# Kernel tuning notes

Measured on AMD Instinct MI355X. Metric: run time of the kernel, lower is better.

The kernel has to match this reference:

```python
import jax, jax.numpy as jnp
import numpy as np

H, W = 256, 256
FRONT_K = 8
ALPHA_T = 1.0 / 255.0
EPS = 1e-8               # transmittance early-stop threshold (meta_f32[4])
BG = (0.0, 0.0, 0.0)     # background color
CHUNK = 128              # gaussians composited per scan step


def setup_inputs() -> dict:
    key = jax.random.key(0)
    k1, k2, k3, k4, k5, k6, k7 = jax.random.split(key, 7)
    B, G = 2, 8192
    # gaussian centers spread over the image plane
    means2d = jax.random.uniform(k1, (B, G, 2), jnp.float32) * jnp.array([W, H], jnp.float32)
    # positive-definite conics (inverse 2D covariance): a, c > 0, |b| < sqrt(a*c)
    a = 0.05 + 0.45 * jax.random.uniform(k2, (B, G), jnp.float32)
    c = 0.05 + 0.45 * jax.random.uniform(k3, (B, G), jnp.float32)
    b = 0.5 * (jax.random.uniform(k4, (B, G), jnp.float32) - 0.5) * jnp.sqrt(a * c)
    conics = jnp.stack([a, b, c], axis=-1)
    colors = jax.random.uniform(k5, (B, G, 3), jnp.float32)
    opacities = jax.random.uniform(k6, (B, G), jnp.float32)
    depths = jax.random.uniform(k7, (B, G), jnp.float32) * 10.0
    return {"means2d": means2d, "conics": conics, "colors": colors,
            "opacities": opacities, "depths": depths}


def _rasterize_one(means2d, conics, colors, opacities, depths):
    # depth sort (stable, front-to-back)
    perm = jnp.argsort(depths, stable=True)
    m = means2d[perm]      # [G,2]
    co = conics[perm]      # [G,3]
    col = colors[perm]     # [G,3]
    op = opacities[perm]   # [G]
    G = m.shape[0]
    n_chunks = G // CHUNK

    px = jnp.arange(W, dtype=jnp.float32) + 0.5  # pixel centers
    py = jnp.arange(H, dtype=jnp.float32) + 0.5
    bg = jnp.asarray(BG, jnp.float32)

    def step(carry, chunk):
        accum, T, count = carry                    # [H,W,3], [H,W], [H,W] int32
        mC, coC, colC, opC = chunk                 # [K,2],[K,3],[K,3],[K]
        dx = px[None, None, :] - mC[:, 0][:, None, None]   # [K,1,W]
        dy = py[None, :, None] - mC[:, 1][:, None, None]   # [K,H,1]
        a = coC[:, 0][:, None, None]
        b = coC[:, 1][:, None, None]
        c = coC[:, 2][:, None, None]
        sigma = 0.5 * (a * dx * dx + c * dy * dy) + b * dx * dy  # [K,H,W]
        alpha = jnp.minimum(opC[:, None, None] * jnp.exp(-sigma), 0.999)
        alpha = jnp.where((sigma >= 0.0) & (alpha >= ALPHA_T), alpha, 0.0)
        kept = (alpha > 0.0).astype(jnp.int32)
        # front_k: only the first FRONT_K contributing gaussians per pixel
        before = count[None] + jnp.cumsum(kept, axis=0) - kept
        alpha = jnp.where(before < FRONT_K, alpha, 0.0)
        kept = (alpha > 0.0).astype(jnp.int32)
        one_m = 1.0 - alpha
        cp = jnp.cumprod(one_m, axis=0)                              # [K,H,W]
        Tc = T[None] * jnp.concatenate([jnp.ones((1, H, W), alpha.dtype), cp[:-1]], 0)
        w = jnp.where(Tc > EPS, Tc * alpha, 0.0)                     # early-stop gate
        accum = accum + jnp.einsum('khw,kc->hwc', w, colC)
        T = T * cp[-1]
        count = count + jnp.sum(kept, axis=0)
        return (accum, T, count), None

    chunks = (m.reshape(n_chunks, CHUNK, 2),
              co.reshape(n_chunks, CHUNK, 3),
              col.reshape(n_chunks, CHUNK, 3),
              op.reshape(n_chunks, CHUNK))
    init = (jnp.zeros((H, W, 3), jnp.float32),
            jnp.ones((H, W), jnp.float32),
            jnp.zeros((H, W), jnp.int32))
    (accum, T, _), _ = jax.lax.scan(step, init, chunks)
    return accum + T[..., None] * bg


def reference(means2d, conics, colors, opacities, depths):
    return jax.vmap(_rasterize_one)(means2d, conics, colors, opacities, depths)
```

## Files before the change

### kernel.cpp

```cpp
#include <hip/hip_runtime.h>
#include <math.h>

#define GN 8192
#define BN 2
#define HN 256
#define WN 256
#define FRONT_K 8
#define EPS_T 1e-8f
#define ALPHA_T (1.0f / 255.0f)
#define TDIM 32
#define NTILE (TDIM * TDIM)
#define CAP 256

__global__ __launch_bounds__(64) void pgr_clear(unsigned* __restrict__ cur)
{
    cur[blockIdx.x * 64 + threadIdx.x] = 0u;
}

__global__ __launch_bounds__(64) void pgr_prep(
    const float* __restrict__ means2d, const float* __restrict__ conics,
    const float* __restrict__ colors, const float* __restrict__ opac,
    const float* __restrict__ depths,
    unsigned* __restrict__ cur, unsigned long long* __restrict__ kent,
    float4* __restrict__ recA, float4* __restrict__ recB,
    float* __restrict__ recC)
{
    int g = blockIdx.x * 64 + threadIdx.x;
    int b = g >> 13, i = g & (GN - 1);
    float2 mxy = reinterpret_cast<const float2*>(means2d)[g];
    float mx = mxy.x, my = mxy.y;
    float ca = conics[3 * g], cb = conics[3 * g + 1], cc = conics[3 * g + 2];
    float r = colors[3 * g], g2 = colors[3 * g + 1], b3 = colors[3 * g + 2];
    float op = opac[g];
    float dep = depths[g];

    float s = (op > 0.f) ? (__logf(255.0f * op) + 1e-4f) : -1.0f;
    if (s < 0.f) return;
    float det = fmaxf(ca * cc - cb * cb, 1e-12f);
    float dxm = sqrtf(2.f * s * cc / det) + 0.02f;
    float dym = sqrtf(2.f * s * ca / det) + 0.02f;
    int x0 = (int)floorf(mx - dxm - 0.5f), x1 = (int)ceilf(mx + dxm - 0.5f);
    int y0 = (int)floorf(my - dym - 0.5f), y1 = (int)ceilf(my + dym - 0.5f);
    if (x1 < 0 || x0 > WN - 1 || y1 < 0 || y0 > HN - 1) return;
    x0 = max(x0, 0); x1 = min(x1, WN - 1);
    y0 = max(y0, 0); y1 = min(y1, HN - 1);
    int tx0 = x0 >> 3, tx1 = x1 >> 3, ty0 = y0 >> 3, ty1 = y1 >> 3;

    unsigned long long key =
        ((unsigned long long)__float_as_uint(dep) << 13) | (unsigned)i;
    float4 A = make_float4(mx, my, ca, cb);
    float4 B = make_float4(cc, op, r, g2);

    for (int ty = ty0; ty <= ty1; ++ty)
        for (int tx = tx0; tx <= tx1; ++tx) {
            int t = b * NTILE + ty * TDIM + tx;
            unsigned pos = atomicAdd(&cur[t], 1u);
            if (pos < CAP) {
                int sl = t * CAP + (int)pos;
                kent[sl] = key;
                recA[sl] = A;
                recB[sl] = B;
                recC[sl] = b3;
            }
        }
}

__device__ __forceinline__ int rank_of(const unsigned long long* s_key,
                                       unsigned long long k, int L)
{
    int rank = 0, j = 0;
    for (; j + 4 <= L; j += 4) {
        unsigned long long k0 = s_key[j], k1 = s_key[j + 1];
        unsigned long long k2 = s_key[j + 2], k3 = s_key[j + 3];
        rank += (int)(k0 < k) + (int)(k1 < k) + (int)(k2 < k) + (int)(k3 < k);
    }
    for (; j < L; ++j) rank += (int)(s_key[j] < k);
    return rank;
}

__global__ __launch_bounds__(64) void pgr_raster(
    const unsigned* __restrict__ cur, const unsigned long long* __restrict__ kent,
    const float4* __restrict__ recA, const float4* __restrict__ recB,
    const float* __restrict__ recC, float* __restrict__ out)
{
    const int b = blockIdx.z;
    const int t = b * NTILE + blockIdx.y * TDIM + blockIdx.x;
    const int tid = threadIdx.x;
    const int tx0 = blockIdx.x * 8, ty0 = blockIdx.y * 8;
    const int lx = tid & 7, ly = tid >> 3;
    const float px = tx0 + lx + 0.5f, py = ty0 + ly + 0.5f;

    __shared__ unsigned long long s_key[CAP];
    __shared__ float4 s_d0[CAP], s_d1[CAP];
    __shared__ float s_d2[CAP];

    const int base = t * CAP;
    unsigned long long myk = kent[base + tid];
    float4 r0 = recA[base + tid];
    float4 r1 = recB[base + tid];
    float r2 = recC[base + tid];
    const int L = min((int)cur[t], CAP);

    if (tid < L) s_key[tid] = myk;
    for (int i = 64 + tid; i < L; i += 64)
        s_key[i] = kent[base + i];
    __syncthreads();

    if (tid < L) {
        int rank = rank_of(s_key, myk, L);
        s_d0[rank] = r0; s_d1[rank] = r1; s_d2[rank] = r2;
    }
    for (int i = 64 + tid; i < L; i += 64) {
        int rank = rank_of(s_key, s_key[i], L);
        s_d0[rank] = recA[base + i];
        s_d1[rank] = recB[base + i];
        s_d2[rank] = recC[base + i];
    }
    __syncthreads();

    float accR = 0.f, accG = 0.f, accB = 0.f, T = 1.f;
    int count = 0;
    bool done = false;

    for (int i0 = 0; i0 < L; i0 += 8) {
        if (__all((int)done)) break;
        float alpha[8], colR[8], colG[8], colB[8];
        bool valid[8];
        #pragma unroll
        for (int k = 0; k < 8; ++k) {
            int idx = i0 + k;
            bool act = (idx < L) && !done;
            int ii = act ? idx : i0;
            float4 d0 = s_d0[ii];
            float4 d1 = s_d1[ii];
            float dx = __fsub_rn(px, d0.x);
            float dy = __fsub_rn(py, d0.y);
            float t1 = __fmul_rn(__fmul_rn(d0.z, dx), dx);
            float t2 = __fmul_rn(__fmul_rn(d1.x, dy), dy);
            float sigma = __fadd_rn(__fmul_rn(0.5f, __fadd_rn(t1, t2)),
                                    __fmul_rn(__fmul_rn(d0.w, dx), dy));
            bool v = act && sigma >= 0.f && sigma <= 5.55f;
            float al = v ? fminf(__fmul_rn(d1.y, __expf(-sigma)), 0.999f) : 0.f;
            valid[k] = v && (al >= ALPHA_T);
            alpha[k] = al;
            colR[k] = d1.z; colG[k] = d1.w; colB[k] = s_d2[ii];
        }
        #pragma unroll
        for (int k = 0; k < 8; ++k) {
            if (valid[k] && !done) {
                float al = alpha[k];
                if (T > EPS_T) {
                    float w = __fmul_rn(T, al);
                    accR += w * colR[k];
                    accG += w * colG[k];
                    accB += w * colB[k];
                }
                T = __fmul_rn(T, __fsub_rn(1.f, al));
                count++;
                if (count >= FRONT_K || T <= EPS_T) done = true;
            }
        }
    }

    int o = ((b * HN + (ty0 + ly)) * WN + (tx0 + lx)) * 3;
    out[o] = accR;
    out[o + 1] = accG;
    out[o + 2] = accB;
}

extern "C" void kernel_launch(void* const* d_in, const int* in_sizes, int n_in,
                              void* d_out, int out_size, void* d_ws, size_t ws_size,
                              hipStream_t stream) {
    const float* means2d = (const float*)d_in[0];
    const float* conics  = (const float*)d_in[1];
    const float* colors  = (const float*)d_in[2];
    const float* opac    = (const float*)d_in[3];
    const float* depths  = (const float*)d_in[4];
    float* out = (float*)d_out;

    const int NSLOT = BN * NTILE * CAP;
    float4*             recA = (float4*)d_ws;
    float4*             recB = recA + NSLOT;
    unsigned long long* kent = (unsigned long long*)(recB + NSLOT);
    float*              recC = (float*)(kent + NSLOT);
    unsigned*           cur  = (unsigned*)(recC + NSLOT);

    pgr_clear<<<(BN * NTILE) / 64, 64, 0, stream>>>(cur);
    pgr_prep<<<(BN * GN) / 64, 64, 0, stream>>>(means2d, conics, colors, opac,
                                                depths, cur, kent, recA, recB, recC);
    pgr_raster<<<dim3(TDIM, TDIM, BN), 64, 0, stream>>>(
        cur, kent, recA, recB, recC, out);
}
```

Measured before the change: 47.91 us.

## Split per-tile gaussian evaluation across four waves with bitmask compositing

The raster block grows from one wave to four. Each thread now loads one sorted entry, so loading and ranking run in a single pass instead of a loop. Each wave tests a quarter of the tile's depth-sorted list and records which gaussians pass the alpha test in a 64-bit mask per pixel. Wave 0 then walks those masks in order and composites only the first FRONT_K contributors, recomputing their alpha. This trades the original early exit for more parallel evaluation across all entries, plus extra sync and a serial tail in one wave.

```diff
diff --git a/kernel.cpp b/kernel.cpp
--- a/kernel.cpp
+++ b/kernel.cpp
@@ -78,7 +78,7 @@
     return rank;
 }
 
-__global__ __launch_bounds__(64) void pgr_raster(
+__global__ __launch_bounds__(256) void pgr_raster(
     const unsigned* __restrict__ cur, const unsigned long long* __restrict__ kent,
     const float4* __restrict__ recA, const float4* __restrict__ recB,
     const float* __restrict__ recC, float* __restrict__ out)
@@ -86,13 +86,15 @@
     const int b = blockIdx.z;
     const int t = b * NTILE + blockIdx.y * TDIM + blockIdx.x;
     const int tid = threadIdx.x;
+    const int wave = tid >> 6, lane = tid & 63;
     const int tx0 = blockIdx.x * 8, ty0 = blockIdx.y * 8;
-    const int lx = tid & 7, ly = tid >> 3;
+    const int lx = lane & 7, ly = lane >> 3;
     const float px = tx0 + lx + 0.5f, py = ty0 + ly + 0.5f;
 
     __shared__ unsigned long long s_key[CAP];
     __shared__ float4 s_d0[CAP], s_d1[CAP];
     __shared__ float s_d2[CAP];
+    __shared__ unsigned long long s_mask[4][64];
 
     const int base = t * CAP;
     unsigned long long myk = kent[base + tid];
@@ -102,35 +104,23 @@
     const int L = min((int)cur[t], CAP);
 
     if (tid < L) s_key[tid] = myk;
-    for (int i = 64 + tid; i < L; i += 64)
-        s_key[i] = kent[base + i];
     __syncthreads();
 
     if (tid < L) {
         int rank = rank_of(s_key, myk, L);
         s_d0[rank] = r0; s_d1[rank] = r1; s_d2[rank] = r2;
     }
-    for (int i = 64 + tid; i < L; i += 64) {
-        int rank = rank_of(s_key, s_key[i], L);
-        s_d0[rank] = recA[base + i];
-        s_d1[rank] = recB[base + i];
-        s_d2[rank] = recC[base + i];
-    }
     __syncthreads();
 
-    float accR = 0.f, accG = 0.f, accB = 0.f, T = 1.f;
-    int count = 0;
-    bool done = false;
-
-    for (int i0 = 0; i0 < L; i0 += 8) {
-        if (__all((int)done)) break;
-        float alpha[8], colR[8], colG[8], colB[8];
-        bool valid[8];
+    const int chunk = (L + 3) >> 2;
+    const int lo = wave * chunk, hi = min(lo + chunk, L);
+    unsigned long long m = 0ull;
+    for (int i0 = lo; i0 < hi; i0 += 8) {
         #pragma unroll
         for (int k = 0; k < 8; ++k) {
             int idx = i0 + k;
-            bool act = (idx < L) && !done;
-            int ii = act ? idx : i0;
+            bool act = idx < hi;
+            int ii = act ? idx : lo;
             float4 d0 = s_d0[ii];
             float4 d1 = s_d1[ii];
             float dx = __fsub_rn(px, d0.x);
@@ -141,31 +131,47 @@
                                     __fmul_rn(__fmul_rn(d0.w, dx), dy));
             bool v = act && sigma >= 0.f && sigma <= 5.55f;
             float al = v ? fminf(__fmul_rn(d1.y, __expf(-sigma)), 0.999f) : 0.f;
-            valid[k] = v && (al >= ALPHA_T);
-            alpha[k] = al;
-            colR[k] = d1.z; colG[k] = d1.w; colB[k] = s_d2[ii];
+            if (al >= ALPHA_T && v) m |= 1ull << (idx - lo);
         }
-        #pragma unroll
-        for (int k = 0; k < 8; ++k) {
-            if (valid[k] && !done) {
-                float al = alpha[k];
+    }
+    s_mask[wave][lane] = m;
+    __syncthreads();
+
+    if (wave == 0) {
+        float accR = 0.f, accG = 0.f, accB = 0.f, T = 1.f;
+        int taken = 0;
+        #pragma unroll 1
+        for (int w = 0; w < 4 && taken < FRONT_K; ++w) {
+            unsigned long long mm = s_mask[w][lane];
+            while (mm && taken < FRONT_K) {
+                int bit = __builtin_ctzll(mm);
+                mm &= mm - 1;
+                int idx = w * chunk + bit;
+                float4 d0 = s_d0[idx];
+                float4 d1 = s_d1[idx];
+                float dx = __fsub_rn(px, d0.x);
+                float dy = __fsub_rn(py, d0.y);
+                float t1 = __fmul_rn(__fmul_rn(d0.z, dx), dx);
+                float t2 = __fmul_rn(__fmul_rn(d1.x, dy), dy);
+                float sigma = __fadd_rn(__fmul_rn(0.5f, __fadd_rn(t1, t2)),
+                                        __fmul_rn(__fmul_rn(d0.w, dx), dy));
+                float al = fminf(__fmul_rn(d1.y, __expf(-sigma)), 0.999f);
                 if (T > EPS_T) {
-                    float w = __fmul_rn(T, al);
-                    accR += w * colR[k];
-                    accG += w * colG[k];
-                    accB += w * colB[k];
+                    float wgt = __fmul_rn(T, al);
+                    accR += wgt * d1.z;
+                    accG += wgt * d1.w;
+                    accB += wgt * s_d2[idx];
                 }
                 T = __fmul_rn(T, __fsub_rn(1.f, al));
-                count++;
-                if (count >= FRONT_K || T <= EPS_T) done = true;
+                ++taken;
+                if (T <= EPS_T) taken = FRONT_K;
             }
         }
+        int o = ((b * HN + (ty0 + ly)) * WN + (tx0 + lx)) * 3;
+        out[o] = accR;
+        out[o + 1] = accG;
+        out[o + 2] = accB;
     }
-
-    int o = ((b * HN + (ty0 + ly)) * WN + (tx0 + lx)) * 3;
-    out[o] = accR;
-    out[o + 1] = accG;
-    out[o + 2] = accB;
 }
 
 extern "C" void kernel_launch(void* const* d_in, const int* in_sizes, int n_in,
@@ -188,6 +194,6 @@
     pgr_clear<<<(BN * NTILE) / 64, 64, 0, stream>>>(cur);
     pgr_prep<<<(BN * GN) / 64, 64, 0, stream>>>(means2d, conics, colors, opac,
                                                 depths, cur, kent, recA, recB, recC);
-    pgr_raster<<<dim3(TDIM, TDIM, BN), 64, 0, stream>>>(
+    pgr_raster<<<dim3(TDIM, TDIM, BN), 256, 0, stream>>>(
         cur, kent, recA, recB, recC, out);
 }
```

Result: no change. 47.40 us (-1.1%).
